# Kernel tuning notes

Measured on AMD Instinct MI355X. Metric: run time of the kernel, lower is better.

Reference implementation:

```python
import math
import jax, jax.numpy as jnp
import numpy as np

B, IN_C, C, FEAT, W, HEADS, EXP = 2, 2, 8, 1024, 512, 8, 4
D = FEAT // HEADS  # head dim = 128


def setup_inputs() -> dict:
    key = jax.random.key(0)
    ks = jax.random.split(key, 16)
    rn = lambda k, shape, s: (jax.random.normal(k, shape, jnp.float32) * s)
    bw = 1.0 / math.sqrt(FEAT)
    return {
        "x": jax.random.normal(ks[0], (B, IN_C, FEAT, W), jnp.float32),
        "embed_w": rn(ks[1], (C, IN_C), 0.5),
        "embed_b": jnp.zeros((C,), jnp.float32),
        "norm1_w": jnp.ones((C, FEAT), jnp.float32),
        "norm1_b": jnp.zeros((C, FEAT), jnp.float32),
        "q_pw": rn(ks[2], (C, FEAT, FEAT), bw),
        "q_cw": rn(ks[3], (C, 1, 1, 3), 0.3),
        "q_cb": jnp.zeros((C,), jnp.float32),
        "k_pw": rn(ks[4], (C, FEAT, FEAT), bw),
        "k_cw": rn(ks[5], (C, 1, 1, 3), 0.3),
        "k_cb": jnp.zeros((C,), jnp.float32),
        "v_pw": rn(ks[6], (C, FEAT, FEAT), bw),
        "v_cw": rn(ks[7], (C, 1, 1, 3), 0.3),
        "v_cb": jnp.zeros((C,), jnp.float32),
        "out_pw": rn(ks[8], (C, FEAT, FEAT), bw),
        "norm2_w": jnp.ones((C, FEAT), jnp.float32),
        "norm2_b": jnp.zeros((C, FEAT), jnp.float32),
        "lin1_pw": rn(ks[9], (C, EXP * FEAT, FEAT), bw),
        "lin1_dw": rn(ks[10], (C, C), 1.0 / math.sqrt(C)),
        "lin2_pw": rn(ks[11], (C, FEAT, EXP * FEAT), 1.0 / math.sqrt(EXP * FEAT)),
    }


def frame_norm(x, w, b, eps=1e-5):
    # LayerNorm over the feature/height axis (axis=2) of [b,c,h,w]
    mu = jnp.mean(x, axis=2, keepdims=True)
    var = jnp.mean((x - mu) ** 2, axis=2, keepdims=True)
    xn = (x - mu) * jax.lax.rsqrt(var + eps)
    return xn * w[None, :, :, None] + b[None, :, :, None]


def mcl_pw(x, wpw):
    # per-channel positionwise linear over feature axis: [b,c,h,w],[c,f,h]->[b,c,f,w]
    return jnp.einsum('bchw,cfh->bcfw', x, wpw)


def dw_conv(x, w, b):
    # depthwise conv with kernel (1,3), padding (0,1) along w axis
    y = jax.lax.conv_general_dilated(
        x, w, window_strides=(1, 1), padding=((0, 0), (1, 1)),
        dimension_numbers=('NCHW', 'OIHW', 'NCHW'),
        feature_group_count=x.shape[1])
    return y + b[None, :, None, None]


def split_heads(x):
    # [b,c,h,w] -> [b,c,heads,w,d]
    b, c, h, w = x.shape
    return x.transpose(0, 1, 3, 2).reshape(b, c, w, HEADS, h // HEADS).transpose(0, 1, 3, 2, 4)


def rotary(x):
    # lucidrains RotaryEmbedding.rotate_queries_or_keys on [..., seq, d]
    d = x.shape[-1]
    seq = x.shape[-2]
    inv_freq = 1.0 / (10000.0 ** (jnp.arange(0, d, 2, dtype=jnp.float32) / d))
    freqs = jnp.arange(seq, dtype=jnp.float32)[:, None] * inv_freq[None, :]  # [seq, d/2]
    freqs = jnp.repeat(freqs, 2, axis=-1)  # interleaved [f0,f0,f1,f1,...]
    cos, sin = jnp.cos(freqs), jnp.sin(freqs)
    x1, x2 = x[..., ::2], x[..., 1::2]
    rot = jnp.stack([-x2, x1], axis=-1).reshape(x.shape)  # rotate_half (interleaved)
    return x * cos + rot * sin


def reference(x, embed_w, embed_b, norm1_w, norm1_b, q_pw, q_cw, q_cb, k_pw, k_cw, k_cb,
              v_pw, v_cw, v_cb, out_pw, norm2_w, norm2_b, lin1_pw, lin1_dw, lin2_pw):
    # embed: 1x1 conv over channel dim
    x = jnp.einsum('bchw,dc->bdhw', x, embed_w) + embed_b[None, :, None, None]
    h = x.shape[2]

    # --- attention block ---
    n1 = frame_norm(x, norm1_w, norm1_b)
    q = rotary(split_heads(dw_conv(mcl_pw(n1, q_pw), q_cw, q_cb)))
    k = rotary(split_heads(dw_conv(mcl_pw(n1, k_pw), k_cw, k_cb)))
    v = split_heads(dw_conv(mcl_pw(n1, v_pw), v_cw, v_cb))
    # NOTE: original scales by sqrt(h) = sqrt(features), not sqrt(head_dim)
    qk = jnp.einsum('bcnqd,bcnkd->bcnqk', q, k) / math.sqrt(h)
    a = jnp.einsum('bcnqk,bcnkd->bcnqd', jax.nn.softmax(qk, axis=-1), v)
    b_, c_, n_, w_, d_ = a.shape
    a = a.transpose(0, 1, 3, 2, 4).reshape(b_, c_, w_, n_ * d_).transpose(0, 1, 3, 2)
    x = x + mcl_pw(a, out_pw)  # dropout is identity in eval

    # --- FFN block ---
    n2 = frame_norm(x, norm2_w, norm2_b)
    hid = mcl_pw(n2, lin1_pw)                     # [b,c,4f,w]
    hid = jnp.einsum('bchw,dc->bdhw', hid, lin1_dw)  # depthwise channel mix
    hid = jnp.maximum(hid, 0.0) ** 2              # squared ReLU
    x = x + mcl_pw(hid, lin2_pw)
    return x
```

## Files before the change

kernel.cpp:

```cpp
#include <hip/hip_runtime.h>

typedef unsigned short u16;
typedef unsigned int u32;
typedef __bf16 bf16x8 __attribute__((ext_vector_type(8)));
typedef float f32x4 __attribute__((ext_vector_type(4)));
typedef unsigned long long ull2 __attribute__((ext_vector_type(2)));
typedef unsigned short u16x4 __attribute__((ext_vector_type(4)));

#define BB 2
#define CC 8
#define FF 1024
#define WW 512
#define NH 8
#define DH 128
#define EFF 4096
#define FW (FF * WW)
#define PE (WW * EFF)

__device__ __forceinline__ u16 f2b(float f) {
  u32 u = __float_as_uint(f);
  u = u + 0x7FFFu + ((u >> 16) & 1u);
  return (u16)(u >> 16);
}
__device__ __forceinline__ float b2f(u16 b) {
  return __uint_as_float(((u32)b) << 16);
}

__device__ __forceinline__ void gload_lds16(const u16* g, u16* l) {
  __builtin_amdgcn_global_load_lds(
      (const __attribute__((address_space(1))) u32*)(uintptr_t)g,
      (__attribute__((address_space(3))) u32*)(uintptr_t)l, 16, 0, 0);
}

__global__ void f2bf(const float* __restrict__ in, u16* __restrict__ out, long n) {
  long i = ((long)blockIdx.x * 256 + threadIdx.x) * 4;
  if (i >= n) return;
  float4 v = *(const float4*)(in + i);
  u16x4 o;
  o[0] = f2b(v.x); o[1] = f2b(v.y); o[2] = f2b(v.z); o[3] = f2b(v.w);
  *(u16x4*)(out + i) = o;
}

__global__ void rope_table(float2* __restrict__ tab) {
  int i = blockIdx.x * 256 + threadIdx.x;
  int w = i >> 6, j = i & 63;
  float invf = powf(10000.f, -(float)(2 * j) / 128.f);
  float fr = (float)w * invf;
  tab[i] = make_float2(cosf(fr), sinf(fr));
}

__global__ void embed_k(const float* __restrict__ x, const float* __restrict__ ew,
                        const float* __restrict__ eb, float* __restrict__ xr) {
  long i = (long)blockIdx.x * 256 + threadIdx.x;
  int w = (int)(i & (WW - 1));
  long t = i >> 9;
  int h = (int)(t & (FF - 1));
  t >>= 10;
  int d = (int)(t & 7);
  int b = (int)(t >> 3);
  long hw = (long)h * WW + w;
  float v0 = x[((long)(b * 2 + 0)) * FW + hw];
  float v1 = x[((long)(b * 2 + 1)) * FW + hw];
  xr[i] = v0 * ew[d * 2] + v1 * ew[d * 2 + 1] + eb[d];
}

__global__ void norm_stats(const float* __restrict__ x, float* __restrict__ mu,
                           float* __restrict__ rs) {
  int z = blockIdx.x;
  int w0 = blockIdx.y * 32;
  int tw = threadIdx.x & 31, th = threadIdx.x >> 5;
  const float* p = x + (long)z * FW + w0 + tw;
  float s = 0.f, s2 = 0.f;
  for (int h = th; h < FF; h += 8) {
    float v = p[(long)h * WW];
    s += v; s2 += v * v;
  }
  __shared__ float ls[8][33], ls2[8][33];
  ls[th][tw] = s; ls2[th][tw] = s2;
  __syncthreads();
  if (th == 0) {
    float a = 0.f, b = 0.f;
#pragma unroll
    for (int j = 0; j < 8; j++) { a += ls[j][tw]; b += ls2[j][tw]; }
    float m = a * (1.f / 1024.f);
    float var = b * (1.f / 1024.f) - m * m;
    mu[z * WW + w0 + tw] = m;
    rs[z * WW + w0 + tw] = rsqrtf(var + 1e-5f);
  }
}

__global__ void norm_apply_t(const float* __restrict__ x, const float* __restrict__ mu,
                             const float* __restrict__ rs, const float* __restrict__ gw,
                             const float* __restrict__ gb, u16* __restrict__ out) {
  int z = blockIdx.x, c = z & 7;
  int w0 = blockIdx.y * 64, h0 = blockIdx.z * 64;
  __shared__ float t[64][65];
  const float* p = x + (long)z * FW;
  int tw = threadIdx.x & 63, tr = threadIdx.x >> 6;
  for (int r = tr; r < 64; r += 4) t[r][tw] = p[(long)(h0 + r) * WW + w0 + tw];
  __syncthreads();
  int hh = threadIdx.x & 63;
  float g = gw[c * FF + h0 + hh], bb = gb[c * FF + h0 + hh];
  for (int r = tr; r < 64; r += 4) {
    int w = w0 + r;
    float m = mu[z * WW + w], q = rs[z * WW + w];
    float v = (t[hh][r] - m) * q * g + bb;
    out[(long)z * FW + (long)w * FF + h0 + hh] = f2b(v);
  }
}

template <int EPI>
__launch_bounds__(256)
__global__ void gemm_nt(const u16* __restrict__ A, const u16* __restrict__ B,
                        u16* __restrict__ Cb, float* Cf, const float* R,
                        int M, int N, int K, int lda, int ldb, int ldc,
                        long sAz, long sBz, long sCz, int aPerC, int bPerC) {
  int z = blockIdx.z;
  const u16* Ap = A + (aPerC ? (long)(z & 7) * sAz : (long)z * sAz);
  const u16* Bp = B + (bPerC ? (long)(z & 7) * sBz : (long)z * sBz);
  long cbase = (long)z * sCz;
  int m0 = blockIdx.x * 128, n0 = blockIdx.y * 128;

  __shared__ __align__(16) u16 As[128 * 32];
  __shared__ __align__(16) u16 Bs[128 * 32];

  int tid = threadIdx.x;
  int lane = tid & 63, wid = tid >> 6;
  int wr = (wid >> 1) * 64, wc = (wid & 1) * 64;
  int lr = lane & 15, kh = lane >> 4;

  f32x4 acc[4][4];
#pragma unroll
  for (int i = 0; i < 4; i++)
#pragma unroll
    for (int j = 0; j < 4; j++) acc[i][j] = (f32x4){0.f, 0.f, 0.f, 0.f};

  int sr = lane >> 2;
  int sc = (lane & 3) * 8;
  const u16* Ag = Ap + (long)(m0 + wid * 32 + sr) * lda + sc;
  const u16* Bg = Bp + (long)(n0 + wid * 32 + sr) * ldb + sc;
  long a16 = (long)16 * lda, b16 = (long)16 * ldb;
  u16* Al0 = As + (wid * 32) * 32;
  u16* Al1 = As + (wid * 32 + 16) * 32;
  u16* Bl0 = Bs + (wid * 32) * 32;
  u16* Bl1 = Bs + (wid * 32 + 16) * 32;

  for (int k0 = 0; k0 < K; k0 += 32) {
    gload_lds16(Ag + k0, Al0);
    gload_lds16(Ag + a16 + k0, Al1);
    gload_lds16(Bg + k0, Bl0);
    gload_lds16(Bg + b16 + k0, Bl1);
    __syncthreads();

    const u16* Ar = As + (wr + lr) * 32 + kh * 8;
    const u16* Br = Bs + (wc + lr) * 32 + kh * 8;
    bf16x8 af[4], bfr[4];
#pragma unroll
    for (int m = 0; m < 4; m++) af[m] = *(const bf16x8*)(Ar + m * 16 * 32);
#pragma unroll
    for (int n = 0; n < 4; n++) bfr[n] = *(const bf16x8*)(Br + n * 16 * 32);
#pragma unroll
    for (int m = 0; m < 4; m++)
#pragma unroll
      for (int n = 0; n < 4; n++)
        acc[m][n] = __builtin_amdgcn_mfma_f32_16x16x32_bf16(af[m], bfr[n], acc[m][n], 0, 0, 0);
    __syncthreads();
  }

  int orow = m0 + wr + kh * 4;
  int ocol = n0 + wc + lr;
#pragma unroll
  for (int m = 0; m < 4; m++)
#pragma unroll
    for (int n = 0; n < 4; n++)
#pragma unroll
      for (int j = 0; j < 4; j++) {
        long idx = cbase + (long)(orow + m * 16 + j) * ldc + (ocol + n * 16);
        float v = acc[m][n][j];
        if (EPI == 0) Cb[idx] = f2b(v);
        else Cf[idx] = R[idx] + v;
      }
}

__global__ void conv_rope(const u16* __restrict__ X, const float* __restrict__ cw,
                          const float* __restrict__ cb, const float2* __restrict__ tab,
                          u16* __restrict__ Oq) {
  int z = blockIdx.x, c = z & 7;
  int f0 = blockIdx.y * 32, w0 = blockIdx.z * 64;
  const u16* p = X + (long)z * FW + (long)f0 * WW;
  float c0 = cw[c * 3], c1 = cw[c * 3 + 1], c2 = cw[c * 3 + 2], cbv = cb[c];
  __shared__ float ct[32][65];
  int cc = threadIdx.x & 63, rr = threadIdx.x >> 6;
  int w = w0 + cc;
  for (int r = rr; r < 32; r += 4) {
    const u16* row = p + (long)r * WW + w;
    float xm = (w > 0) ? b2f(row[-1]) : 0.f;
    float x0 = b2f(row[0]);
    float xp = (w < WW - 1) ? b2f(row[1]) : 0.f;
    ct[r][cc] = c0 * xm + c1 * x0 + c2 * xp + cbv;
  }
  __syncthreads();
  int dd = threadIdx.x & 31, wi = threadIdx.x >> 5;
  int nh = f0 >> 7, d0 = f0 & 127;
  int dg = d0 + dd;
  long ob = ((long)(z * NH + nh)) * WW * DH;
  for (int r2 = wi; r2 < 64; r2 += 8) {
    int wg = w0 + r2;
    float2 cs = tab[(long)wg * 64 + (dg >> 1)];
    float xv = ct[dd][r2];
    float v;
    if ((dg & 1) == 0) v = xv * cs.x - ct[dd + 1][r2] * cs.y;
    else               v = xv * cs.x + ct[dd - 1][r2] * cs.y;
    Oq[ob + (long)wg * DH + dg] = f2b(v);
  }
}

__global__ void conv_v(const u16* __restrict__ X, const float* __restrict__ cw,
                       const float* __restrict__ cb, u16* __restrict__ Ov) {
  long i = (long)blockIdx.x * 256 + threadIdx.x;
  int w = (int)(i & (WW - 1));
  long t = i >> 9;
  int z = (int)(t >> 10);
  int c = z & 7;
  const u16* row = X + i;
  float xm = (w > 0) ? b2f(row[-1]) : 0.f;
  float x0 = b2f(row[0]);
  float xp = (w < WW - 1) ? b2f(row[1]) : 0.f;
  Ov[i] = f2b(cw[c * 3] * xm + cw[c * 3 + 1] * x0 + cw[c * 3 + 2] * xp + cb[c]);
}

__launch_bounds__(256)
__global__ void attn_k(const u16* __restrict__ Q, const u16* __restrict__ Kt,
                       const u16* __restrict__ Vt, u16* __restrict__ O) {
  int z = blockIdx.x, n = blockIdx.y, qt = blockIdx.z;
  long hbase = ((long)(z * NH + n)) * WW * DH;
  const u16* Qp = Q + hbase + (long)qt * 32 * DH;
  const u16* Kp = Kt + hbase;
  const u16* Vp = Vt + (long)z * FW + (long)n * DH * WW;

  __shared__ __align__(16) float S[32][516];
  __shared__ __align__(16) u16 Qs[32 * 136];

  int tid = threadIdx.x, lane = tid & 63, wid = tid >> 6;
  int lr = lane & 15, kh = lane >> 4;

#pragma unroll
  for (int p = 0; p < 2; p++) {
    int idx = p * 256 + tid;
    int r = idx >> 4, ch = (idx & 15) * 8;
    *(ull2*)(Qs + r * 136 + ch) = *(const ull2*)(Qp + (long)r * DH + ch);
  }
  __syncthreads();

  f32x4 sacc[2][8];
#pragma unroll
  for (int m = 0; m < 2; m++)
#pragma unroll
    for (int nn = 0; nn < 8; nn++) sacc[m][nn] = (f32x4){0.f, 0.f, 0.f, 0.f};

  const u16* Qr = Qs + lr * 136 + kh * 8;
  const u16* Kr = Kp + (long)(wid * 128 + lr) * DH + kh * 8;
#pragma unroll
  for (int ks = 0; ks < 4; ks++) {
    bf16x8 qa0 = *(const bf16x8*)(Qr + ks * 32);
    bf16x8 qa1 = *(const bf16x8*)(Qr + 16 * 136 + ks * 32);
#pragma unroll
    for (int nn = 0; nn < 8; nn++) {
      bf16x8 kb = *(const bf16x8*)(Kr + (long)nn * 16 * DH + ks * 32);
      sacc[0][nn] = __builtin_amdgcn_mfma_f32_16x16x32_bf16(qa0, kb, sacc[0][nn], 0, 0, 0);
      sacc[1][nn] = __builtin_amdgcn_mfma_f32_16x16x32_bf16(qa1, kb, sacc[1][nn], 0, 0, 0);
    }
  }
#pragma unroll
  for (int m = 0; m < 2; m++)
#pragma unroll
    for (int nn = 0; nn < 8; nn++) {
      int col = wid * 128 + nn * 16 + lr;
      int row = m * 16 + kh * 4;
#pragma unroll
      for (int j = 0; j < 4; j++) S[row + j][col] = sacc[m][nn][j] * 0.03125f;
    }
  __syncthreads();

  int rowi = tid >> 3, sub = tid & 7;
  float mx = -1e30f;
  for (int j = sub; j < 512; j += 8) mx = fmaxf(mx, S[rowi][j]);
#pragma unroll
  for (int o = 1; o < 8; o <<= 1) mx = fmaxf(mx, __shfl_xor(mx, o));
  float sm = 0.f;
  for (int j = sub; j < 512; j += 8) {
    float e = __expf(S[rowi][j] - mx);
    S[rowi][j] = e; sm += e;
  }
#pragma unroll
  for (int o = 1; o < 8; o <<= 1) sm += __shfl_xor(sm, o);
  float inv = 1.f / sm;
  for (int j = sub; j < 512; j += 8) S[rowi][j] *= inv;
  __syncthreads();

  f32x4 oacc[2][2];
#pragma unroll
  for (int m = 0; m < 2; m++)
#pragma unroll
    for (int nn = 0; nn < 2; nn++) oacc[m][nn] = (f32x4){0.f, 0.f, 0.f, 0.f};

  const u16* Vr = Vp + (long)(wid * 32 + lr) * WW;
#pragma unroll 4
  for (int ks = 0; ks < 16; ks++) {
    int kwb = ks * 32 + kh * 8;
    bf16x8 pa[2];
#pragma unroll
    for (int m = 0; m < 2; m++) {
      const float* Pr = &S[m * 16 + lr][kwb];
      f32x4 plo = *(const f32x4*)Pr;
      f32x4 phi = *(const f32x4*)(Pr + 4);
      union { bf16x8 v; u16 s[8]; } pu;
      pu.s[0] = f2b(plo[0]); pu.s[1] = f2b(plo[1]);
      pu.s[2] = f2b(plo[2]); pu.s[3] = f2b(plo[3]);
      pu.s[4] = f2b(phi[0]); pu.s[5] = f2b(phi[1]);
      pu.s[6] = f2b(phi[2]); pu.s[7] = f2b(phi[3]);
      pa[m] = pu.v;
    }
#pragma unroll
    for (int nn = 0; nn < 2; nn++) {
      bf16x8 vb = *(const bf16x8*)(Vr + (long)nn * 16 * WW + kwb);
      oacc[0][nn] = __builtin_amdgcn_mfma_f32_16x16x32_bf16(pa[0], vb, oacc[0][nn], 0, 0, 0);
      oacc[1][nn] = __builtin_amdgcn_mfma_f32_16x16x32_bf16(pa[1], vb, oacc[1][nn], 0, 0, 0);
    }
  }

  long ob = (long)z * WW * FF + (long)n * 128;
#pragma unroll
  for (int m = 0; m < 2; m++)
#pragma unroll
    for (int nn = 0; nn < 2; nn++)
#pragma unroll
      for (int j = 0; j < 4; j++) {
        int qw = qt * 32 + m * 16 + kh * 4 + j;
        int d = wid * 32 + nn * 16 + lr;
        O[ob + (long)qw * FF + d] = f2b(oacc[m][nn][j]);
      }
}

__global__ void mix_sq(const u16* __restrict__ H, const float* __restrict__ dwm,
                       u16* __restrict__ O) {
  __shared__ float wsm[64];
  if (threadIdx.x < 64) wsm[threadIdx.x] = dwm[threadIdx.x];
  __syncthreads();
  long ti = (long)blockIdx.x * 256 + threadIdx.x;
  int e4 = (int)(ti & 1023);
  int w = (int)((ti >> 10) & (WW - 1));
  int b = (int)(ti >> 19);
  long off = (long)(b * 8) * PE + (long)w * EFF + e4 * 4;
  float v[8][4];
#pragma unroll
  for (int c = 0; c < 8; c++) {
    u16x4 hv = *(const u16x4*)(H + off + (long)c * PE);
    v[c][0] = b2f(hv[0]); v[c][1] = b2f(hv[1]);
    v[c][2] = b2f(hv[2]); v[c][3] = b2f(hv[3]);
  }
#pragma unroll
  for (int d = 0; d < 8; d++) {
    u16x4 ov;
#pragma unroll
    for (int q = 0; q < 4; q++) {
      float s = 0.f;
#pragma unroll
      for (int c = 0; c < 8; c++) s += v[c][q] * wsm[d * 8 + c];
      s = fmaxf(s, 0.f);
      ov[q] = f2b(s * s);
    }
    *(u16x4*)(O + off + (long)d * PE) = ov;
  }
}

extern "C" void kernel_launch(void* const* d_in, const int* in_sizes, int n_in,
                              void* d_out, int out_size, void* d_ws, size_t ws_size,
                              hipStream_t stream) {
  const float* x_in = (const float*)d_in[0];
  const float* ew   = (const float*)d_in[1];
  const float* eb   = (const float*)d_in[2];
  const float* n1w  = (const float*)d_in[3];
  const float* n1b  = (const float*)d_in[4];
  const float* q_pw = (const float*)d_in[5];
  const float* q_cw = (const float*)d_in[6];
  const float* q_cb = (const float*)d_in[7];
  const float* k_pw = (const float*)d_in[8];
  const float* k_cw = (const float*)d_in[9];
  const float* k_cb = (const float*)d_in[10];
  const float* v_pw = (const float*)d_in[11];
  const float* v_cw = (const float*)d_in[12];
  const float* v_cb = (const float*)d_in[13];
  const float* o_pw = (const float*)d_in[14];
  const float* n2w  = (const float*)d_in[15];
  const float* n2b  = (const float*)d_in[16];
  const float* l1pw = (const float*)d_in[17];
  const float* l1dw = (const float*)d_in[18];
  const float* l2pw = (const float*)d_in[19];
  float* out = (float*)d_out;

  if (ws_size < 184877056ULL) return;

  char* ws = (char*)d_ws;
  float*  xr  = (float*)(ws + 0L);
  u16*    nt  = (u16*)(ws + 33554432L);
  float*  mu  = (float*)(ws + 50331648L);
  float*  rs  = (float*)(ws + 50364416L);
  float2* tab = (float2*)(ws + 50397184L);
  char* pool  = ws + 50659328L;
  const long SLOT = 16777216L;
  u16* S0 = (u16*)(pool + 0 * SLOT);
  u16* S1 = (u16*)(pool + 1 * SLOT);
  u16* S2 = (u16*)(pool + 2 * SLOT);
  u16* S3 = (u16*)(pool + 3 * SLOT);
  u16* S4 = (u16*)(pool + 4 * SLOT);
  u16* S5 = (u16*)(pool + 5 * SLOT);

  rope_table<<<128, 256, 0, stream>>>(tab);
  embed_k<<<32768, 256, 0, stream>>>(x_in, ew, eb, xr);

  norm_stats<<<dim3(16, 16), 256, 0, stream>>>(xr, mu, rs);
  norm_apply_t<<<dim3(16, 8, 16), 256, 0, stream>>>(xr, mu, rs, n1w, n1b, nt);

  dim3 gq(8, 4, 16);
  f2bf<<<8192, 256, 0, stream>>>(q_pw, S0, 8388608L);
  gemm_nt<0><<<gq, 256, 0, stream>>>(S0, nt, S3, nullptr, nullptr,
      1024, 512, 1024, 1024, 1024, 512, 1048576L, 524288L, 524288L, 1, 0);
  f2bf<<<8192, 256, 0, stream>>>(k_pw, S1, 8388608L);
  gemm_nt<0><<<gq, 256, 0, stream>>>(S1, nt, S4, nullptr, nullptr,
      1024, 512, 1024, 1024, 1024, 512, 1048576L, 524288L, 524288L, 1, 0);
  f2bf<<<8192, 256, 0, stream>>>(v_pw, S2, 8388608L);
  gemm_nt<0><<<gq, 256, 0, stream>>>(S2, nt, S5, nullptr, nullptr,
      1024, 512, 1024, 1024, 1024, 512, 1048576L, 524288L, 524288L, 1, 0);

  conv_rope<<<dim3(16, 32, 8), 256, 0, stream>>>(S3, q_cw, q_cb, tab, S0);
  conv_rope<<<dim3(16, 32, 8), 256, 0, stream>>>(S4, k_cw, k_cb, tab, S1);
  conv_v<<<32768, 256, 0, stream>>>(S5, v_cw, v_cb, S2);

  attn_k<<<dim3(16, 8, 16), 256, 0, stream>>>(S0, S1, S2, S3);

  f2bf<<<8192, 256, 0, stream>>>(o_pw, S4, 8388608L);
  gemm_nt<1><<<gq, 256, 0, stream>>>(S4, S3, nullptr, xr, xr,
      1024, 512, 1024, 1024, 1024, 512, 1048576L, 524288L, 524288L, 1, 0);

  norm_stats<<<dim3(16, 16), 256, 0, stream>>>(xr, mu, rs);
  norm_apply_t<<<dim3(16, 8, 16), 256, 0, stream>>>(xr, mu, rs, n2w, n2b, nt);

  u16* wl1  = S0;
  u16* hidT = S4;
  f2bf<<<32768, 256, 0, stream>>>(l1pw, wl1, 33554432L);
  gemm_nt<0><<<dim3(4, 32, 16), 256, 0, stream>>>(nt, wl1, hidT, nullptr, nullptr,
      512, 4096, 1024, 1024, 1024, 4096, 524288L, 4194304L, 2097152L, 0, 1);

  u16* h2T = S0;
  mix_sq<<<4096, 256, 0, stream>>>(hidT, l1dw, h2T);

  u16* wl2 = S4;
  f2bf<<<32768, 256, 0, stream>>>(l2pw, wl2, 33554432L);
  gemm_nt<1><<<gq, 256, 0, stream>>>(wl2, h2T, nullptr, out, xr,
      1024, 512, 4096, 4096, 4096, 512, 4194304L, 2097152L, 524288L, 1, 0);
}
```

Baseline: 1.095 ms.

## Merge QKV GEMMs, swizzle block order by channel, split-K with atomics

Replaces the batched gemm_nt with gemm_sw, which uses a flat 1D grid. The low bits of the block index select the channel, so blocks that share the same per-channel weight are scheduled together for L2 reuse. The three Q/K/V projections are merged into a single launch. The output and lin2 projections use split-K (2 and 4 ways) with atomicAdd into fp32 accumulators that are pre-seeded with the residual; for lin2 this needs an added device-to-device memcpy. This trades more parallelism and fewer launches for atomic traffic and nondeterministic summation order.

```diff
diff --git a/kernel.cpp b/kernel.cpp
--- a/kernel.cpp
+++ b/kernel.cpp
@@ -109,17 +109,50 @@
   }
 }
 
-template <int EPI>
+template <int MODE, int NK>
 __launch_bounds__(256)
-__global__ void gemm_nt(const u16* __restrict__ A, const u16* __restrict__ B,
-                        u16* __restrict__ Cb, float* Cf, const float* R,
-                        int M, int N, int K, int lda, int ldb, int ldc,
-                        long sAz, long sBz, long sCz, int aPerC, int bPerC) {
-  int z = blockIdx.z;
-  const u16* Ap = A + (aPerC ? (long)(z & 7) * sAz : (long)z * sAz);
-  const u16* Bp = B + (bPerC ? (long)(z & 7) * sBz : (long)z * sBz);
-  long cbase = (long)z * sCz;
-  int m0 = blockIdx.x * 128, n0 = blockIdx.y * 128;
+__global__ void gemm_sw(const u16* __restrict__ W0, const u16* __restrict__ W1,
+                        const u16* __restrict__ W2, const u16* __restrict__ X,
+                        u16* O0, u16* O1, u16* O2, float* OF,
+                        int K, int lda, int ldb, int ldc,
+                        long sWz, long sXz, long sOz) {
+  int bid = blockIdx.x;
+  int g = bid & 7, t = bid >> 3;
+  const u16 *Ap, *Bp;
+  u16* Cb = nullptr;
+  float* Cfz = nullptr;
+  int m0, n0, k_lo, k_hi;
+  if (MODE == 0) {
+    int p = t / 64, r = t - p * 64;
+    int h = r >> 5, q = r & 31;
+    n0 = (q >> 3) << 7; m0 = (q & 7) << 7;
+    int z = g + (h << 3);
+    const u16* W = (p == 0) ? W0 : (p == 1) ? W1 : W2;
+    u16* O = (p == 0) ? O0 : (p == 1) ? O1 : O2;
+    Ap = W + (long)g * sWz;
+    Bp = X + (long)z * sXz;
+    Cb = O + (long)z * sOz;
+    k_lo = 0; k_hi = K;
+  } else if (MODE == 1) {
+    int n = t >> 3, r = t & 7;
+    int h = r >> 2, m = r & 3;
+    n0 = n << 7; m0 = m << 7;
+    int z = g + (h << 3);
+    Ap = X + (long)z * sXz;
+    Bp = W0 + (long)g * sWz;
+    Cb = O0 + (long)z * sOz;
+    k_lo = 0; k_hi = K;
+  } else {
+    int kq = t >> 6, r = t & 63;
+    int h = r >> 5, q = r & 31;
+    n0 = (q >> 3) << 7; m0 = (q & 7) << 7;
+    int z = g + (h << 3);
+    Ap = W0 + (long)g * sWz;
+    Bp = X + (long)z * sXz;
+    Cfz = OF + (long)z * sOz;
+    int kc = K / NK;
+    k_lo = kq * kc; k_hi = k_lo + kc;
+  }
 
   __shared__ __align__(16) u16 As[128 * 32];
   __shared__ __align__(16) u16 Bs[128 * 32];
@@ -145,7 +178,7 @@
   u16* Bl0 = Bs + (wid * 32) * 32;
   u16* Bl1 = Bs + (wid * 32 + 16) * 32;
 
-  for (int k0 = 0; k0 < K; k0 += 32) {
+  for (int k0 = k_lo; k0 < k_hi; k0 += 32) {
     gload_lds16(Ag + k0, Al0);
     gload_lds16(Ag + a16 + k0, Al1);
     gload_lds16(Bg + k0, Bl0);
@@ -175,10 +208,10 @@
     for (int n = 0; n < 4; n++)
 #pragma unroll
       for (int j = 0; j < 4; j++) {
-        long idx = cbase + (long)(orow + m * 16 + j) * ldc + (ocol + n * 16);
+        long idx = (long)(orow + m * 16 + j) * ldc + (ocol + n * 16);
         float v = acc[m][n][j];
-        if (EPI == 0) Cb[idx] = f2b(v);
-        else Cf[idx] = R[idx] + v;
+        if (MODE == 2) atomicAdd(&Cfz[idx], v);
+        else Cb[idx] = f2b(v);
       }
 }
 
@@ -422,16 +455,11 @@
   norm_stats<<<dim3(16, 16), 256, 0, stream>>>(xr, mu, rs);
   norm_apply_t<<<dim3(16, 8, 16), 256, 0, stream>>>(xr, mu, rs, n1w, n1b, nt);
 
-  dim3 gq(8, 4, 16);
   f2bf<<<8192, 256, 0, stream>>>(q_pw, S0, 8388608L);
-  gemm_nt<0><<<gq, 256, 0, stream>>>(S0, nt, S3, nullptr, nullptr,
-      1024, 512, 1024, 1024, 1024, 512, 1048576L, 524288L, 524288L, 1, 0);
   f2bf<<<8192, 256, 0, stream>>>(k_pw, S1, 8388608L);
-  gemm_nt<0><<<gq, 256, 0, stream>>>(S1, nt, S4, nullptr, nullptr,
-      1024, 512, 1024, 1024, 1024, 512, 1048576L, 524288L, 524288L, 1, 0);
   f2bf<<<8192, 256, 0, stream>>>(v_pw, S2, 8388608L);
-  gemm_nt<0><<<gq, 256, 0, stream>>>(S2, nt, S5, nullptr, nullptr,
-      1024, 512, 1024, 1024, 1024, 512, 1048576L, 524288L, 524288L, 1, 0);
+  gemm_sw<0, 1><<<1536, 256, 0, stream>>>(S0, S1, S2, nt, S3, S4, S5, nullptr,
+      1024, 1024, 1024, 512, 1048576L, 524288L, 524288L);
 
   conv_rope<<<dim3(16, 32, 8), 256, 0, stream>>>(S3, q_cw, q_cb, tab, S0);
   conv_rope<<<dim3(16, 32, 8), 256, 0, stream>>>(S4, k_cw, k_cb, tab, S1);
@@ -440,8 +468,9 @@
   attn_k<<<dim3(16, 8, 16), 256, 0, stream>>>(S0, S1, S2, S3);
 
   f2bf<<<8192, 256, 0, stream>>>(o_pw, S4, 8388608L);
-  gemm_nt<1><<<gq, 256, 0, stream>>>(S4, S3, nullptr, xr, xr,
-      1024, 512, 1024, 1024, 1024, 512, 1048576L, 524288L, 524288L, 1, 0);
+  gemm_sw<2, 2><<<1024, 256, 0, stream>>>(S4, nullptr, nullptr, S3,
+      nullptr, nullptr, nullptr, xr,
+      1024, 1024, 1024, 512, 1048576L, 524288L, 524288L);
 
   norm_stats<<<dim3(16, 16), 256, 0, stream>>>(xr, mu, rs);
   norm_apply_t<<<dim3(16, 8, 16), 256, 0, stream>>>(xr, mu, rs, n2w, n2b, nt);
@@ -449,14 +478,17 @@
   u16* wl1  = S0;
   u16* hidT = S4;
   f2bf<<<32768, 256, 0, stream>>>(l1pw, wl1, 33554432L);
-  gemm_nt<0><<<dim3(4, 32, 16), 256, 0, stream>>>(nt, wl1, hidT, nullptr, nullptr,
-      512, 4096, 1024, 1024, 1024, 4096, 524288L, 4194304L, 2097152L, 0, 1);
+  gemm_sw<1, 1><<<2048, 256, 0, stream>>>(wl1, nullptr, nullptr, nt,
+      hidT, nullptr, nullptr, nullptr,
+      1024, 1024, 1024, 4096, 4194304L, 524288L, 2097152L);
 
   u16* h2T = S0;
   mix_sq<<<4096, 256, 0, stream>>>(hidT, l1dw, h2T);
 
   u16* wl2 = S4;
   f2bf<<<32768, 256, 0, stream>>>(l2pw, wl2, 33554432L);
-  gemm_nt<1><<<gq, 256, 0, stream>>>(wl2, h2T, nullptr, out, xr,
-      1024, 512, 4096, 4096, 4096, 512, 4194304L, 2097152L, 524288L, 1, 0);
-}
+  hipMemcpyAsync(out, xr, 33554432L, hipMemcpyDeviceToDevice, stream);
+  gemm_sw<2, 4><<<2048, 256, 0, stream>>>(wl2, nullptr, nullptr, h2T,
+      nullptr, nullptr, nullptr, out,
+      4096, 4096, 4096, 512, 4194304L, 2097152L, 524288L);
+}
```

New measurement: 1.122 ms. +2.5%, slower.
